# Optimization experiments

Measured on AMD Instinct MI355X. Metric: run time of the kernel, lower is better.

Reference implementation:

```python
import jax, jax.numpy as jnp
import numpy as np

# Network geometry: 8 layers x 524288 buckets, 8 spigots per bucket (uniform).
L_LAYERS = 8
B_PER_LAYER = 524288
NB = L_LAYERS * B_PER_LAYER      # total buckets = 4_194_304
NS = 8                           # spigots per bucket
G = 9.8                          # gravity constant from module


def setup_inputs() -> dict:
    key = jax.random.key(0)
    k1, k2, k3, k4 = jax.random.split(key, 4)
    # Head starts above all spigot heights (initial_head_in_buckets ~ 2) so h > 0.
    H = 2.0 + jax.random.uniform(k1, (NB,), dtype=jnp.float32)
    # S[..., 0] = spigot height in (0,1); S[..., 1] = spigot area in (0,1).
    S = jax.random.uniform(k2, (NB, NS, 2), dtype=jnp.float32)
    # theta flattened in (layer, bucket, spigot) order -> plain reshape to [NB, NS].
    theta = jax.random.uniform(k3, (NB * NS,), dtype=jnp.float32)
    # precip_into_network_at_update (scalar), unit_precip = 6.0 scale.
    precip = jax.random.uniform(k4, (), dtype=jnp.float32) * 6.0
    return {"H": H, "S": S, "theta": theta, "precip": precip}


def reference(H, S, theta, precip):
    # --- update_spigot_outflow (vectorized over layers/buckets/spigots) ---
    th = theta.reshape(NB, NS)                      # triple loop == reshape
    h = jnp.maximum(0.0, H[:, None] - S[:, :, 0])   # head above spigot
    flow_rate_modifier = 0.5 * (jnp.tanh(h) + 1.0)
    v = th * jnp.sqrt(2.0 * G * h) * flow_rate_modifier
    s_q = v * S[:, :, 1]                            # [NB, NS] spigot outflows

    # --- update_network_fluxes (upstream precip distribution) ---
    outflows = jnp.sum(s_q, axis=1)                 # [NB]
    # inflows[1:] = outflows[:-1]; inflows[0] = precip (upstream)
    inflows = jnp.concatenate([precip[None].astype(H.dtype), outflows[:-1]])

    # --- update_head_in_buckets ---
    H_new = H + inflows - outflows

    # --- set_network_outflow: total outflow of last layer's buckets ---
    network_outflow = jnp.sum(s_q[NB - B_PER_LAYER:])

    return H_new, s_q, network_outflow
```

## Files before the change

kernel.cpp:

```cpp
#include <hip/hip_runtime.h>

#define NL 8
#define BPL 524288
#define NB (NL * BPL)
#define NS 8
#define GRAV 9.8f

__device__ __forceinline__ float spigot_q(float th, float hgt, float area, float Hb) {
    const float h   = fmaxf(0.0f, Hb - hgt);
    const float e   = __expf(-2.0f * h);
    const float mod = __builtin_amdgcn_rcpf(1.0f + e);
    return th * __builtin_amdgcn_sqrtf(2.0f * GRAV * h) * mod * area;
}

__global__ __launch_bounds__(256) void fused_kernel(
    const float* __restrict__ H,
    const float* __restrict__ S,
    const float* __restrict__ theta,
    const float* __restrict__ precip,
    float* __restrict__ s_q,
    float* __restrict__ H_new,
    float* __restrict__ net_out)
{
    const int bucket = blockIdx.x * 256 + threadIdx.x;
    const int lane   = threadIdx.x & 63;
    const int wbase  = bucket - lane;

    float  pth = 0.0f, pH = 0.0f, pre = 0.0f;
    float2 psv = make_float2(0.0f, 0.0f);
    if (wbase > 0) {
        if (lane < 8) {
            const int pidx = (wbase - 1) * 8 + lane;
            pth = theta[pidx];
            psv = reinterpret_cast<const float2*>(S)[pidx];
            pH  = H[wbase - 1];
        }
    } else if (lane == 0) {
        pre = precip[0];
    }

    const float  Hb = H[bucket];
    const float4 t0 = reinterpret_cast<const float4*>(theta)[bucket * 2];
    const float4 t1 = reinterpret_cast<const float4*>(theta)[bucket * 2 + 1];
    const float4 s0 = reinterpret_cast<const float4*>(S)[bucket * 4];
    const float4 s1 = reinterpret_cast<const float4*>(S)[bucket * 4 + 1];
    const float4 s2 = reinterpret_cast<const float4*>(S)[bucket * 4 + 2];
    const float4 s3 = reinterpret_cast<const float4*>(S)[bucket * 4 + 3];

    const float q0 = spigot_q(t0.x, s0.x, s0.y, Hb);
    const float q1 = spigot_q(t0.y, s0.z, s0.w, Hb);
    const float q2 = spigot_q(t0.z, s1.x, s1.y, Hb);
    const float q3 = spigot_q(t0.w, s1.z, s1.w, Hb);
    const float q4 = spigot_q(t1.x, s2.x, s2.y, Hb);
    const float q5 = spigot_q(t1.y, s2.z, s2.w, Hb);
    const float q6 = spigot_q(t1.z, s3.x, s3.y, Hb);
    const float q7 = spigot_q(t1.w, s3.z, s3.w, Hb);

    reinterpret_cast<float4*>(s_q)[bucket * 2]     = make_float4(q0, q1, q2, q3);
    reinterpret_cast<float4*>(s_q)[bucket * 2 + 1] = make_float4(q4, q5, q6, q7);

    const float of = ((q0 + q1) + (q2 + q3)) + ((q4 + q5) + (q6 + q7));

    float pq = spigot_q(pth, psv.x, psv.y, pH);
    pq += __shfl_xor(pq, 1);
    pq += __shfl_xor(pq, 2);
    pq += __shfl_xor(pq, 4);

    const float prev   = __shfl_up(of, 1);
    const float inflow = (lane == 0) ? ((wbase == 0) ? pre : pq) : prev;

    H_new[bucket] = Hb + inflow - of;

    if (bucket >= NB - BPL) {
        float part = of;
        part += __shfl_xor(part, 1);
        part += __shfl_xor(part, 2);
        part += __shfl_xor(part, 4);
        part += __shfl_xor(part, 8);
        part += __shfl_xor(part, 16);
        part += __shfl_xor(part, 32);

        __shared__ float wsum[4];
        if (lane == 0) wsum[threadIdx.x >> 6] = part;
        __syncthreads();
        if (threadIdx.x == 0) {
            atomicAdd(net_out, (wsum[0] + wsum[1]) + (wsum[2] + wsum[3]));
        }
    }
}

extern "C" void kernel_launch(void* const* d_in, const int* in_sizes, int n_in,
                              void* d_out, int out_size, void* d_ws, size_t ws_size,
                              hipStream_t stream) {
    const float* H      = (const float*)d_in[0];
    const float* S      = (const float*)d_in[1];
    const float* theta  = (const float*)d_in[2];
    const float* precip = (const float*)d_in[3];

    float* out     = (float*)d_out;
    float* H_new   = out;
    float* s_q     = out + NB;
    float* net_out = out + NB + (size_t)NB * NS;

    hipMemsetAsync(net_out, 0, sizeof(float), stream);

    fused_kernel<<<NB / 256, 256, 0, stream>>>(
        H, S, theta, precip, s_q, H_new, net_out);
}
```

Measured before the change: 492.6 us.

## Split each bucket across four threads and use nontemporal stores

```diff
diff --git a/kernel.cpp b/kernel.cpp
--- a/kernel.cpp
+++ b/kernel.cpp
@@ -13,6 +13,12 @@
     return th * __builtin_amdgcn_sqrtf(2.0f * GRAV * h) * mod * area;
 }
 
+__device__ __forceinline__ void nt_store_f2(float* p, float2 v) {
+    unsigned long long bits;
+    __builtin_memcpy(&bits, &v, 8);
+    __builtin_nontemporal_store(bits, reinterpret_cast<unsigned long long*>(p));
+}
+
 __global__ __launch_bounds__(256) void fused_kernel(
     const float* __restrict__ H,
     const float* __restrict__ S,
@@ -22,59 +28,49 @@
     float* __restrict__ H_new,
     float* __restrict__ net_out)
 {
-    const int bucket = blockIdx.x * 256 + threadIdx.x;
+    const int t      = blockIdx.x * 256 + threadIdx.x;
     const int lane   = threadIdx.x & 63;
-    const int wbase  = bucket - lane;
+    const int bucket = t >> 2;
+    const int pb     = ((t - lane) >> 2) - 1;
 
-    float  pth = 0.0f, pH = 0.0f, pre = 0.0f;
-    float2 psv = make_float2(0.0f, 0.0f);
-    if (wbase > 0) {
-        if (lane < 8) {
-            const int pidx = (wbase - 1) * 8 + lane;
-            pth = theta[pidx];
-            psv = reinterpret_cast<const float2*>(S)[pidx];
-            pH  = H[wbase - 1];
+    float2 pt = make_float2(0.0f, 0.0f);
+    float4 ps = make_float4(0.0f, 0.0f, 0.0f, 0.0f);
+    float  pH = 0.0f, pre = 0.0f;
+    if (pb >= 0) {
+        if (lane < 4) {
+            pt = reinterpret_cast<const float2*>(theta)[pb * 4 + lane];
+            ps = reinterpret_cast<const float4*>(S)[pb * 4 + lane];
+            pH = H[pb];
         }
     } else if (lane == 0) {
         pre = precip[0];
     }
 
     const float  Hb = H[bucket];
-    const float4 t0 = reinterpret_cast<const float4*>(theta)[bucket * 2];
-    const float4 t1 = reinterpret_cast<const float4*>(theta)[bucket * 2 + 1];
-    const float4 s0 = reinterpret_cast<const float4*>(S)[bucket * 4];
-    const float4 s1 = reinterpret_cast<const float4*>(S)[bucket * 4 + 1];
-    const float4 s2 = reinterpret_cast<const float4*>(S)[bucket * 4 + 2];
-    const float4 s3 = reinterpret_cast<const float4*>(S)[bucket * 4 + 3];
+    const float2 tv = reinterpret_cast<const float2*>(theta)[t];
+    const float4 sv = reinterpret_cast<const float4*>(S)[t];
 
-    const float q0 = spigot_q(t0.x, s0.x, s0.y, Hb);
-    const float q1 = spigot_q(t0.y, s0.z, s0.w, Hb);
-    const float q2 = spigot_q(t0.z, s1.x, s1.y, Hb);
-    const float q3 = spigot_q(t0.w, s1.z, s1.w, Hb);
-    const float q4 = spigot_q(t1.x, s2.x, s2.y, Hb);
-    const float q5 = spigot_q(t1.y, s2.z, s2.w, Hb);
-    const float q6 = spigot_q(t1.z, s3.x, s3.y, Hb);
-    const float q7 = spigot_q(t1.w, s3.z, s3.w, Hb);
+    const float q0 = spigot_q(tv.x, sv.x, sv.y, Hb);
+    const float q1 = spigot_q(tv.y, sv.z, sv.w, Hb);
 
-    reinterpret_cast<float4*>(s_q)[bucket * 2]     = make_float4(q0, q1, q2, q3);
-    reinterpret_cast<float4*>(s_q)[bucket * 2 + 1] = make_float4(q4, q5, q6, q7);
+    nt_store_f2(s_q + (size_t)t * 2, make_float2(q0, q1));
 
-    const float of = ((q0 + q1) + (q2 + q3)) + ((q4 + q5) + (q6 + q7));
+    float of = q0 + q1;
+    of += __shfl_xor(of, 1);
+    of += __shfl_xor(of, 2);
 
-    float pq = spigot_q(pth, psv.x, psv.y, pH);
+    float pq = spigot_q(pt.x, ps.x, ps.y, pH) + spigot_q(pt.y, ps.z, ps.w, pH);
     pq += __shfl_xor(pq, 1);
     pq += __shfl_xor(pq, 2);
-    pq += __shfl_xor(pq, 4);
 
-    const float prev   = __shfl_up(of, 1);
-    const float inflow = (lane == 0) ? ((wbase == 0) ? pre : pq) : prev;
+    const float prev = __shfl_up(of, 4);
+    if ((lane & 3) == 0) {
+        const float inflow = (lane == 0) ? ((pb < 0) ? pre : pq) : prev;
+        __builtin_nontemporal_store(Hb + inflow - of, &H_new[bucket]);
+    }
 
-    H_new[bucket] = Hb + inflow - of;
-
-    if (bucket >= NB - BPL) {
+    if (t >= (NB - BPL) * 4) {
         float part = of;
-        part += __shfl_xor(part, 1);
-        part += __shfl_xor(part, 2);
         part += __shfl_xor(part, 4);
         part += __shfl_xor(part, 8);
         part += __shfl_xor(part, 16);
@@ -104,6 +100,6 @@
 
     hipMemsetAsync(net_out, 0, sizeof(float), stream);
 
-    fused_kernel<<<NB / 256, 256, 0, stream>>>(
+    fused_kernel<<<(NB * 4) / 256, 256, 0, stream>>>(
         H, S, theta, precip, s_q, H_new, net_out);
 }
```

Result: slower. 567.7 us (+15.2%).
